# Kernel optimization log

Measured on AMD Instinct MI355X. Metric: run time of the kernel, lower is better.

The kernel has to match this reference:

```python
import jax, jax.numpy as jnp
import numpy as np

T, B = 2048, 128
H = 128          # hidden_size
QH = 1024        # query_hidden_size
NF = 32          # num_convolution_filters
K = 31           # convolution_filter_size (odd, same padding)


def setup_inputs() -> dict:
    key = jax.random.key(0)
    ks = jax.random.split(key, 10)
    encoded_tokens = jax.random.normal(ks[0], (T, B, H), dtype=jnp.float32)
    tokens_mask = jax.random.randint(ks[1], (B, T), 0, 2).astype(jnp.bool_)
    query = jax.random.normal(ks[2], (1, B, QH), dtype=jnp.float32)
    cumulative_alignment = jax.random.uniform(ks[3], (B, T), dtype=jnp.float32)
    # parameters
    conv_w = jax.random.normal(ks[4], (NF, 1, K), dtype=jnp.float32) * 0.1   # Conv1d weight [out,in,k]
    conv_b = jnp.zeros((NF,), dtype=jnp.float32)
    Wq = jax.random.normal(ks[5], (H, QH), dtype=jnp.float32) * (1.0 / np.sqrt(QH))
    bq = jnp.zeros((H,), dtype=jnp.float32)
    Wa = jax.random.normal(ks[6], (H, NF), dtype=jnp.float32) * (1.0 / np.sqrt(NF))
    ba = jnp.zeros((H,), dtype=jnp.float32)
    score_w = jax.random.normal(ks[7], (H,), dtype=jnp.float32) * (1.0 / np.sqrt(H))  # xavier-ish
    score_b = jnp.zeros((H,), dtype=jnp.float32)
    return dict(encoded_tokens=encoded_tokens, tokens_mask=tokens_mask, query=query,
                cumulative_alignment=cumulative_alignment, conv_w=conv_w, conv_b=conv_b,
                Wq=Wq, bq=bq, Wa=Wa, ba=ba, score_w=score_w, score_b=score_b)


def reference(encoded_tokens, tokens_mask, query, cumulative_alignment,
              conv_w, conv_b, Wq, bq, Wa, ba, score_w, score_b):
    # location features: Conv1d over cumulative alignment, same padding
    loc = jax.lax.conv_general_dilated(
        cumulative_alignment[:, None, :], conv_w,
        window_strides=(1,), padding=[((K - 1) // 2, (K - 1) // 2)],
        dimension_numbers=('NCH', 'OIH', 'NCH'))  # [B, NF, T]
    loc = loc + conv_b[None, :, None]
    loc = jnp.transpose(loc, (2, 0, 1))                        # [T, B, NF]
    loc = jnp.einsum('tbf,hf->tbh', loc, Wa) + ba              # [T, B, H]
    q = jnp.einsum('obq,hq->obh', query, Wq) + bq              # [1, B, H]
    # additive score: tanh of fused elementwise sum, then project to scalar
    score = jnp.tanh(encoded_tokens + q + loc + score_b)       # [T, B, H]
    s = jnp.einsum('tbh,h->bt', score, score_w)                # [B, T]
    s = jnp.where(tokens_mask, -jnp.inf, s)
    alignment = jax.nn.softmax(s, axis=1)                      # [B, T]
    context = jnp.einsum('bt,tbh->bh', alignment, encoded_tokens)  # [B, H]
    cumulative_alignment = cumulative_alignment + alignment
    return context, cumulative_alignment, alignment
```

## Files before the change

kernel.cpp:

```cpp
#include <hip/hip_runtime.h>
#include <stdint.h>

#define T_DIM 2048
#define B_DIM 128
#define H_DIM 128
#define QH_DIM 1024
#define NF 32
#define KW 31
#define TT 128
#define NTILE (T_DIM / TT)

#define NEG_INF (-__builtin_inff())

__device__ __forceinline__ float fast_tanh(float x) {
    float e = __expf(2.0f * x);
    return 1.0f - 2.0f * __builtin_amdgcn_rcpf(1.0f + e);
}

__global__ void k0_G(const float* __restrict__ Wa, const float* __restrict__ conv_w,
                     float* __restrict__ G) {
    int gid = blockIdx.x * blockDim.x + threadIdx.x;
    if (gid >= H_DIM * KW) return;
    int k = gid >> 7, h = gid & 127;
    float acc = 0.0f;
    #pragma unroll
    for (int f = 0; f < NF; ++f) acc = fmaf(Wa[h * NF + f], conv_w[f * KW + k], acc);
    G[gid] = acc;
}

__global__ __launch_bounds__(512)
void k1_query(const float* __restrict__ query, const float* __restrict__ Wq,
              const float* __restrict__ bq, const float* __restrict__ Wa,
              const float* __restrict__ conv_b, const float* __restrict__ ba,
              const float* __restrict__ score_b, float* __restrict__ qb) {
    const int b = blockIdx.x, tid = threadIdx.x;
    const int h = tid & 127, qtr = tid >> 7;
    __shared__ __align__(16) float qrow[QH_DIM];
    __shared__ float partial[512];
    for (int i = tid; i < QH_DIM; i += 512) qrow[i] = query[b * QH_DIM + i];
    __syncthreads();
    const float4* wq4 = (const float4*)(Wq + (size_t)h * QH_DIM + qtr * 256);
    const float4* q4 = (const float4*)(qrow + qtr * 256);
    float acc = 0.0f;
    #pragma unroll 4
    for (int j = 0; j < 64; ++j) {
        float4 w = wq4[j], q = q4[j];
        acc += w.x * q.x + w.y * q.y + w.z * q.z + w.w * q.w;
    }
    if (qtr == 0) {
        float cb = bq[h] + ba[h] + score_b[h];
        #pragma unroll
        for (int f = 0; f < NF; ++f) cb = fmaf(Wa[h * NF + f], conv_b[f], cb);
        acc += cb;
    }
    partial[tid] = acc;
    __syncthreads();
    if (tid < 128) qb[b * H_DIM + h] = partial[h] + partial[h + 128] + partial[h + 256] + partial[h + 384];
}

__global__ __launch_bounds__(256, 4)
void k2_score(const float* __restrict__ enc, const float* __restrict__ cum,
              const void* __restrict__ mask, const float* __restrict__ G,
              const float* __restrict__ qb, const float* __restrict__ score_w,
              float* __restrict__ s_out, float* __restrict__ o_part,
              float* __restrict__ ml_part) {
    const int b = blockIdx.x;
    const int tile = blockIdx.y;
    const int t0 = tile * TT;
    const int tid = threadIdx.x;
    const int l = tid & 63, wv = tid >> 6;

    __shared__ float Gs[KW * H_DIM];
    __shared__ float cw[TT + KW - 1];
    __shared__ float mbias[TT];
    __shared__ float oc[4][H_DIM];
    __shared__ float mwl[4], lwl[4];

    {
        uint32_t u = ((const uint32_t*)mask)[l];
        unsigned long long hi = __ballot(u > 1u);
        unsigned long long nf = __ballot(u != 0u && u != 0x3f800000u);
        int layout = (hi == 0ull) ? 0 : ((nf == 0ull) ? 2 : 1);
        if (tid < TT) {
            int idx = b * T_DIM + t0 + tid;
            bool m;
            if (layout == 0)      m = ((const int32_t*)mask)[idx] != 0;
            else if (layout == 1) m = ((const uint8_t*)mask)[idx] != 0;
            else                  m = ((const float*)mask)[idx] != 0.0f;
            mbias[tid] = m ? NEG_INF : 0.0f;
        }
    }
    for (int i = tid; i < KW * H_DIM; i += 256) Gs[i] = G[i];
    if (tid < TT + KW - 1) {
        int t = t0 - (KW / 2) + tid;
        cw[tid] = (t >= 0 && t < T_DIM) ? cum[b * T_DIM + t] : 0.0f;
    }
    __syncthreads();

    const float2 base = *(const float2*)(qb + b * H_DIM + 2 * l);
    const float2 w2 = *(const float2*)(score_w + 2 * l);

    float m_w = NEG_INF, l_w = 0.0f;
    float ox = 0.0f, oy = 0.0f;

    #pragma unroll
    for (int si = 0; si < 4; ++si) {
        const int cbase = wv * 32 + si * 8;
        float2 acc[8];
        #pragma unroll
        for (int it = 0; it < 8; ++it) acc[it] = base;

        {
            float tp[23];
            #pragma unroll
            for (int j = 0; j < 23; ++j) tp[j] = cw[cbase + j];
            #pragma unroll
            for (int k = 0; k < 16; ++k) {
                const float2 gk = *(const float2*)(&Gs[k * H_DIM + 2 * l]);
                #pragma unroll
                for (int it = 0; it < 8; ++it) {
                    acc[it].x = fmaf(gk.x, tp[k + it], acc[it].x);
                    acc[it].y = fmaf(gk.y, tp[k + it], acc[it].y);
                }
            }
        }
        {
            float tp[22];
            #pragma unroll
            for (int j = 0; j < 22; ++j) tp[j] = cw[cbase + 16 + j];
            #pragma unroll
            for (int k = 16; k < 31; ++k) {
                const float2 gk = *(const float2*)(&Gs[k * H_DIM + 2 * l]);
                #pragma unroll
                for (int it = 0; it < 8; ++it) {
                    acc[it].x = fmaf(gk.x, tp[k - 16 + it], acc[it].x);
                    acc[it].y = fmaf(gk.y, tp[k - 16 + it], acc[it].y);
                }
            }
        }

        const float* ep = enc + ((size_t)(t0 + cbase) * B_DIM + b) * H_DIM + 2 * l;
        float ex[8], ey[8], s_arr[8];
        #pragma unroll
        for (int it = 0; it < 8; ++it) {
            const float2 e2 = *(const float2*)(ep + (size_t)it * (B_DIM * H_DIM));
            ex[it] = e2.x; ey[it] = e2.y;
            float p = w2.x * fast_tanh(acc[it].x + e2.x)
                    + w2.y * fast_tanh(acc[it].y + e2.y);
            #pragma unroll
            for (int m = 32; m >= 1; m >>= 1) p += __shfl_xor(p, m, 64);
            s_arr[it] = p + mbias[cbase + it];
        }
        float sv = s_arr[0];
        #pragma unroll
        for (int it = 1; it < 8; ++it) sv = (l == it) ? s_arr[it] : sv;
        if (l < 8) s_out[b * T_DIM + t0 + cbase + l] = sv;
        float m8 = s_arr[0];
        #pragma unroll
        for (int it = 1; it < 8; ++it) m8 = fmaxf(m8, s_arr[it]);
        const float m_new = fmaxf(m_w, m8);
        const float m_use = (m_new == NEG_INF) ? 0.0f : m_new;
        const float alpha = __expf(m_w - m_use);
        float lsum = 0.0f, osx = 0.0f, osy = 0.0f;
        #pragma unroll
        for (int it = 0; it < 8; ++it) {
            const float e = __expf(s_arr[it] - m_use);
            lsum += e;
            osx = fmaf(e, ex[it], osx);
            osy = fmaf(e, ey[it], osy);
        }
        l_w = fmaf(l_w, alpha, lsum);
        ox = fmaf(ox, alpha, osx);
        oy = fmaf(oy, alpha, osy);
        m_w = m_new;
    }

    oc[wv][2 * l] = ox;
    oc[wv][2 * l + 1] = oy;
    if (l == 0) { mwl[wv] = m_w; lwl[wv] = l_w; }
    __syncthreads();
    if (tid < H_DIM) {
        const float mb = fmaxf(fmaxf(mwl[0], mwl[1]), fmaxf(mwl[2], mwl[3]));
        const float mu = (mb == NEG_INF) ? 0.0f : mb;
        const float b0 = __expf(mwl[0] - mu), b1 = __expf(mwl[1] - mu);
        const float b2 = __expf(mwl[2] - mu), b3 = __expf(mwl[3] - mu);
        const float o = oc[0][tid] * b0 + oc[1][tid] * b1 + oc[2][tid] * b2 + oc[3][tid] * b3;
        const int tbase = b * NTILE + tile;
        o_part[tbase * H_DIM + tid] = o;
        if (tid == 0) {
            ml_part[tbase * 2] = mb;
            ml_part[tbase * 2 + 1] = lwl[0] * b0 + lwl[1] * b1 + lwl[2] * b2 + lwl[3] * b3;
        }
    }
}

__global__ __launch_bounds__(256)
void k5_final(float* __restrict__ s_align, const float* __restrict__ cum_in,
              float* __restrict__ cum_out, const float* __restrict__ o_part,
              const float* __restrict__ ml_part, float* __restrict__ ctx) {
    const int b = blockIdx.x, tid = threadIdx.x;
    __shared__ float sm[NTILE], sl[NTILE], sb[NTILE];
    if (tid < NTILE) {
        sm[tid] = ml_part[(b * NTILE + tid) * 2];
        sl[tid] = ml_part[(b * NTILE + tid) * 2 + 1];
    }
    __syncthreads();
    float M = sm[0];
    #pragma unroll
    for (int i = 1; i < NTILE; ++i) M = fmaxf(M, sm[i]);
    const float M_use = (M == NEG_INF) ? 0.0f : M;
    if (tid < NTILE) sb[tid] = __expf(sm[tid] - M_use);
    __syncthreads();
    float L = 0.0f;
    #pragma unroll
    for (int i = 0; i < NTILE; ++i) L = fmaf(sl[i], sb[i], L);
    const float invL = 1.0f / L;
    if (tid < H_DIM) {
        float o = 0.0f;
        #pragma unroll
        for (int i = 0; i < NTILE; ++i)
            o = fmaf(o_part[(b * NTILE + i) * H_DIM + tid], sb[i], o);
        ctx[b * H_DIM + tid] = o * invL;
    }
    #pragma unroll
    for (int j = 0; j < 8; ++j) {
        const int idx = b * T_DIM + tid + j * 256;
        const float a = __expf(s_align[idx] - M_use) * invL;
        s_align[idx] = a;
        cum_out[idx] = cum_in[idx] + a;
    }
}

extern "C" void kernel_launch(void* const* d_in, const int* in_sizes, int n_in,
                              void* d_out, int out_size, void* d_ws, size_t ws_size,
                              hipStream_t stream) {
    const float* enc     = (const float*)d_in[0];
    const void*  mask    = d_in[1];
    const float* query   = (const float*)d_in[2];
    const float* cum     = (const float*)d_in[3];
    const float* conv_w  = (const float*)d_in[4];
    const float* conv_b  = (const float*)d_in[5];
    const float* Wq      = (const float*)d_in[6];
    const float* bq      = (const float*)d_in[7];
    const float* Wa      = (const float*)d_in[8];
    const float* ba      = (const float*)d_in[9];
    const float* score_w = (const float*)d_in[10];
    const float* score_b = (const float*)d_in[11];

    float* ctx_out   = (float*)d_out;
    float* cum_out   = ctx_out + B_DIM * H_DIM;
    float* align_out = cum_out + B_DIM * T_DIM;

    float* G      = (float*)d_ws;
    float* qb     = G + 4096;
    float* o_part = qb + B_DIM * H_DIM;
    float* ml     = o_part + B_DIM * NTILE * H_DIM;

    k0_G<<<16, 256, 0, stream>>>(Wa, conv_w, G);
    k1_query<<<B_DIM, 512, 0, stream>>>(query, Wq, bq, Wa, conv_b, ba, score_b, qb);
    k2_score<<<dim3(B_DIM, NTILE), 256, 0, stream>>>(enc, cum, mask, G, qb, score_w,
                                                     align_out, o_part, ml);
    k5_final<<<B_DIM, 256, 0, stream>>>(align_out, cum, cum_out, o_part, ml, ctx_out);
}
```

Baseline: 262.7 us.

## Precompute padded cumulative and mask bias, widen score tile, DPP wave reduction

Adds a prep kernel that writes a zero-padded copy of the cumulative alignment and a float mask bias to workspace, so the score kernel no longer stages them through shared memory or detects the mask layout per block. The score kernel now processes 16 timesteps per chunk instead of 8 and reuses 46 register-held conv inputs across all 31 taps. It prefetches all 16 encoder rows before the convolution, uses packed two-wide FMAs, and replaces the shuffle butterfly reduction with DPP row ops plus readlane. The cost is an extra kernel launch, extra global traffic for the padded buffers, and higher register pressure at 4 blocks per SIMD. The tp reads from global memory may also be less efficient than the earlier shared-memory reads.

```diff
diff --git a/kernel.cpp b/kernel.cpp
--- a/kernel.cpp
+++ b/kernel.cpp
@@ -9,12 +9,50 @@
 #define KW 31
 #define TT 128
 #define NTILE (T_DIM / TT)
+#define CPAD_ROW (T_DIM + 32)
 
 #define NEG_INF (-__builtin_inff())
+
+typedef float v2f __attribute__((ext_vector_type(2)));
 
 __device__ __forceinline__ float fast_tanh(float x) {
     float e = __expf(2.0f * x);
     return 1.0f - 2.0f * __builtin_amdgcn_rcpf(1.0f + e);
+}
+
+template <int CTRL>
+__device__ __forceinline__ float dpp_add(float x) {
+    int m = __builtin_amdgcn_update_dpp(0, __float_as_int(x), CTRL, 0xf, 0xf, true);
+    return x + __int_as_float(m);
+}
+__device__ __forceinline__ float wave_sum64(float x) {
+    x = dpp_add<0x111>(x);
+    x = dpp_add<0x112>(x);
+    x = dpp_add<0x114>(x);
+    x = dpp_add<0x118>(x);
+    x = dpp_add<0x142>(x);
+    x = dpp_add<0x143>(x);
+    return __int_as_float(__builtin_amdgcn_readlane(__float_as_int(x), 63));
+}
+
+__global__ __launch_bounds__(256)
+void k_prep(const float* __restrict__ cum, const void* __restrict__ mask,
+            float* __restrict__ cpad, float* __restrict__ mbias) {
+    const int gid = blockIdx.x * 256 + threadIdx.x;
+    const int b = gid >> 11, t = gid & 2047;
+    const int l = threadIdx.x & 63;
+    uint32_t u = ((const uint32_t*)mask)[l];
+    unsigned long long hi = __ballot(u > 1u);
+    unsigned long long nf = __ballot(u != 0u && u != 0x3f800000u);
+    int layout = (hi == 0ull) ? 0 : ((nf == 0ull) ? 2 : 1);
+    bool m;
+    if (layout == 0)      m = ((const int32_t*)mask)[gid] != 0;
+    else if (layout == 1) m = ((const uint8_t*)mask)[gid] != 0;
+    else                  m = ((const float*)mask)[gid] != 0.0f;
+    mbias[gid] = m ? NEG_INF : 0.0f;
+    cpad[b * CPAD_ROW + 16 + t] = cum[gid];
+    if (t < 16) cpad[b * CPAD_ROW + t] = 0.0f;
+    else if (t >= T_DIM - 16) cpad[b * CPAD_ROW + 32 + t] = 0.0f;
 }
 
 __global__ void k0_G(const float* __restrict__ Wa, const float* __restrict__ conv_w,
@@ -59,8 +97,8 @@
 }
 
 __global__ __launch_bounds__(256, 4)
-void k2_score(const float* __restrict__ enc, const float* __restrict__ cum,
-              const void* __restrict__ mask, const float* __restrict__ G,
+void k2_score(const float* __restrict__ enc, const float* __restrict__ cpad,
+              const float* __restrict__ mbias, const float* __restrict__ G,
               const float* __restrict__ qb, const float* __restrict__ score_w,
               float* __restrict__ s_out, float* __restrict__ o_part,
               float* __restrict__ ml_part) {
@@ -70,113 +108,82 @@
     const int tid = threadIdx.x;
     const int l = tid & 63, wv = tid >> 6;
 
-    __shared__ float Gs[KW * H_DIM];
-    __shared__ float cw[TT + KW - 1];
-    __shared__ float mbias[TT];
+    __shared__ v2f Gs[KW * 64];
     __shared__ float oc[4][H_DIM];
     __shared__ float mwl[4], lwl[4];
 
-    {
-        uint32_t u = ((const uint32_t*)mask)[l];
-        unsigned long long hi = __ballot(u > 1u);
-        unsigned long long nf = __ballot(u != 0u && u != 0x3f800000u);
-        int layout = (hi == 0ull) ? 0 : ((nf == 0ull) ? 2 : 1);
-        if (tid < TT) {
-            int idx = b * T_DIM + t0 + tid;
-            bool m;
-            if (layout == 0)      m = ((const int32_t*)mask)[idx] != 0;
-            else if (layout == 1) m = ((const uint8_t*)mask)[idx] != 0;
-            else                  m = ((const float*)mask)[idx] != 0.0f;
-            mbias[tid] = m ? NEG_INF : 0.0f;
-        }
-    }
-    for (int i = tid; i < KW * H_DIM; i += 256) Gs[i] = G[i];
-    if (tid < TT + KW - 1) {
-        int t = t0 - (KW / 2) + tid;
-        cw[tid] = (t >= 0 && t < T_DIM) ? cum[b * T_DIM + t] : 0.0f;
-    }
-    __syncthreads();
-
-    const float2 base = *(const float2*)(qb + b * H_DIM + 2 * l);
-    const float2 w2 = *(const float2*)(score_w + 2 * l);
+    for (int i = tid; i < KW * 64; i += 256) Gs[i] = ((const v2f*)G)[i];
+    __syncthreads();
+
+    const v2f base = *(const v2f*)(qb + b * H_DIM + 2 * l);
+    const v2f w2 = *(const v2f*)(score_w + 2 * l);
+    const float* crow = cpad + b * CPAD_ROW;
+    const float* mrow = mbias + b * T_DIM;
 
     float m_w = NEG_INF, l_w = 0.0f;
-    float ox = 0.0f, oy = 0.0f;
-
-    #pragma unroll
-    for (int si = 0; si < 4; ++si) {
-        const int cbase = wv * 32 + si * 8;
-        float2 acc[8];
-        #pragma unroll
-        for (int it = 0; it < 8; ++it) acc[it] = base;
-
-        {
-            float tp[23];
+    v2f o_w = {0.0f, 0.0f};
+
+    #pragma unroll
+    for (int c = 0; c < 2; ++c) {
+        const int tb = t0 + wv * 32 + c * 16;
+
+        float tp[46];
+        #pragma unroll
+        for (int j = 0; j < 46; ++j) tp[j] = crow[tb + j + 1];
+
+        const float* ep = enc + ((size_t)tb * B_DIM + b) * H_DIM + 2 * l;
+        v2f ee[16];
+        #pragma unroll
+        for (int it = 0; it < 16; ++it)
+            ee[it] = *(const v2f*)(ep + (size_t)it * (B_DIM * H_DIM));
+
+        v2f acc[16];
+        #pragma unroll
+        for (int it = 0; it < 16; ++it) acc[it] = base;
+        #pragma unroll
+        for (int k = 0; k < KW; ++k) {
+            const v2f g = Gs[k * 64 + l];
             #pragma unroll
-            for (int j = 0; j < 23; ++j) tp[j] = cw[cbase + j];
-            #pragma unroll
-            for (int k = 0; k < 16; ++k) {
-                const float2 gk = *(const float2*)(&Gs[k * H_DIM + 2 * l]);
-                #pragma unroll
-                for (int it = 0; it < 8; ++it) {
-                    acc[it].x = fmaf(gk.x, tp[k + it], acc[it].x);
-                    acc[it].y = fmaf(gk.y, tp[k + it], acc[it].y);
-                }
+            for (int it = 0; it < 16; ++it) {
+                const float cc = tp[k + it];
+                acc[it] = __builtin_elementwise_fma(g, (v2f){cc, cc}, acc[it]);
             }
         }
-        {
-            float tp[22];
-            #pragma unroll
-            for (int j = 0; j < 22; ++j) tp[j] = cw[cbase + 16 + j];
-            #pragma unroll
-            for (int k = 16; k < 31; ++k) {
-                const float2 gk = *(const float2*)(&Gs[k * H_DIM + 2 * l]);
-                #pragma unroll
-                for (int it = 0; it < 8; ++it) {
-                    acc[it].x = fmaf(gk.x, tp[k - 16 + it], acc[it].x);
-                    acc[it].y = fmaf(gk.y, tp[k - 16 + it], acc[it].y);
-                }
-            }
-        }
-
-        const float* ep = enc + ((size_t)(t0 + cbase) * B_DIM + b) * H_DIM + 2 * l;
-        float ex[8], ey[8], s_arr[8];
-        #pragma unroll
-        for (int it = 0; it < 8; ++it) {
-            const float2 e2 = *(const float2*)(ep + (size_t)it * (B_DIM * H_DIM));
-            ex[it] = e2.x; ey[it] = e2.y;
-            float p = w2.x * fast_tanh(acc[it].x + e2.x)
-                    + w2.y * fast_tanh(acc[it].y + e2.y);
-            #pragma unroll
-            for (int m = 32; m >= 1; m >>= 1) p += __shfl_xor(p, m, 64);
-            s_arr[it] = p + mbias[cbase + it];
-        }
-        float sv = s_arr[0];
-        #pragma unroll
-        for (int it = 1; it < 8; ++it) sv = (l == it) ? s_arr[it] : sv;
-        if (l < 8) s_out[b * T_DIM + t0 + cbase + l] = sv;
-        float m8 = s_arr[0];
-        #pragma unroll
-        for (int it = 1; it < 8; ++it) m8 = fmaxf(m8, s_arr[it]);
-        const float m_new = fmaxf(m_w, m8);
+
+        float su[16];
+        #pragma unroll
+        for (int it = 0; it < 16; ++it) {
+            v2f a = acc[it] + ee[it];
+            float p = w2.x * fast_tanh(a.x) + w2.y * fast_tanh(a.y);
+            su[it] = wave_sum64(p) + mrow[tb + it];
+        }
+
+        float sv = su[0];
+        #pragma unroll
+        for (int it = 1; it < 16; ++it) sv = (l == it) ? su[it] : sv;
+        if (l < 16) s_out[b * T_DIM + tb + l] = sv;
+
+        float mc = su[0];
+        #pragma unroll
+        for (int it = 1; it < 16; ++it) mc = fmaxf(mc, su[it]);
+        const float m_new = fmaxf(m_w, mc);
         const float m_use = (m_new == NEG_INF) ? 0.0f : m_new;
         const float alpha = __expf(m_w - m_use);
-        float lsum = 0.0f, osx = 0.0f, osy = 0.0f;
-        #pragma unroll
-        for (int it = 0; it < 8; ++it) {
-            const float e = __expf(s_arr[it] - m_use);
+        float lsum = 0.0f;
+        v2f osum = {0.0f, 0.0f};
+        #pragma unroll
+        for (int it = 0; it < 16; ++it) {
+            const float e = __expf(su[it] - m_use);
             lsum += e;
-            osx = fmaf(e, ex[it], osx);
-            osy = fmaf(e, ey[it], osy);
+            osum = __builtin_elementwise_fma((v2f){e, e}, ee[it], osum);
         }
         l_w = fmaf(l_w, alpha, lsum);
-        ox = fmaf(ox, alpha, osx);
-        oy = fmaf(oy, alpha, osy);
+        o_w = __builtin_elementwise_fma(o_w, (v2f){alpha, alpha}, osum);
         m_w = m_new;
     }
 
-    oc[wv][2 * l] = ox;
-    oc[wv][2 * l + 1] = oy;
+    oc[wv][2 * l] = o_w.x;
+    oc[wv][2 * l + 1] = o_w.y;
     if (l == 0) { mwl[wv] = m_w; lwl[wv] = l_w; }
     __syncthreads();
     if (tid < H_DIM) {
@@ -255,10 +262,13 @@
     float* qb     = G + 4096;
     float* o_part = qb + B_DIM * H_DIM;
     float* ml     = o_part + B_DIM * NTILE * H_DIM;
-
+    float* cpad   = ml + 4096;
+    float* mb     = cpad + B_DIM * CPAD_ROW;
+
+    k_prep<<<B_DIM * T_DIM / 256, 256, 0, stream>>>(cum, mask, cpad, mb);
     k0_G<<<16, 256, 0, stream>>>(Wa, conv_w, G);
     k1_query<<<B_DIM, 512, 0, stream>>>(query, Wq, bq, Wa, conv_b, ba, score_b, qb);
-    k2_score<<<dim3(B_DIM, NTILE), 256, 0, stream>>>(enc, cum, mask, G, qb, score_w,
+    k2_score<<<dim3(B_DIM, NTILE), 256, 0, stream>>>(enc, cpad, mb, G, qb, score_w,
                                                      align_out, o_part, ml);
     k5_final<<<B_DIM, 256, 0, stream>>>(align_out, cum, cum_out, o_part, ml, ctx_out);
 }
```

Result: no change. 264.5 us (+0.7%).

## Remap score kernel to one thread per timestep with LDS-staged encoder tiles

Applied to the files above, without the earlier changes.

The score kernel now assigns one timestep per thread over 256-step tiles instead of lanes across hidden units. Encoder chunks of 32 hidden units are staged through a padded shared-memory tile with register prefetch of the next chunk. The conv-projection weights are read from global memory in a pair-interleaved layout rather than copied to shared memory. Per-wave softmax reductions use DPP, and the context sum reloads the encoder rows in a second pass. This removes per-timestep cross-lane shuffle reductions and the shared G copy, at the cost of reading the encoder twice and adding more barriers and register pressure.

```diff
diff --git a/kernel.cpp b/kernel.cpp
--- a/kernel.cpp
+++ b/kernel.cpp
@@ -7,25 +7,51 @@
 #define QH_DIM 1024
 #define NF 32
 #define KW 31
-#define TT 128
-#define NTILE (T_DIM / TT)
+#define TB 256
+#define NTILE (T_DIM / TB)
+#define HC 32
+#define TROW 33
 
 #define NEG_INF (-__builtin_inff())
+
+typedef float v2f __attribute__((ext_vector_type(2)));
 
 __device__ __forceinline__ float fast_tanh(float x) {
     float e = __expf(2.0f * x);
     return 1.0f - 2.0f * __builtin_amdgcn_rcpf(1.0f + e);
 }
 
+template <int C>
+__device__ __forceinline__ float dpp_add(float x) {
+    int m = __builtin_amdgcn_update_dpp(0, __float_as_int(x), C, 0xf, 0xf, true);
+    return x + __int_as_float(m);
+}
+template <int C>
+__device__ __forceinline__ float dpp_max(float x) {
+    int m = __builtin_amdgcn_update_dpp(__float_as_int(x), __float_as_int(x), C, 0xf, 0xf, false);
+    return fmaxf(x, __int_as_float(m));
+}
+__device__ __forceinline__ float wave_sum64(float x) {
+    x = dpp_add<0x111>(x); x = dpp_add<0x112>(x); x = dpp_add<0x114>(x); x = dpp_add<0x118>(x);
+    x = dpp_add<0x142>(x); x = dpp_add<0x143>(x);
+    return __int_as_float(__builtin_amdgcn_readlane(__float_as_int(x), 63));
+}
+__device__ __forceinline__ float wave_max64(float x) {
+    x = dpp_max<0x111>(x); x = dpp_max<0x112>(x); x = dpp_max<0x114>(x); x = dpp_max<0x118>(x);
+    x = dpp_max<0x142>(x); x = dpp_max<0x143>(x);
+    return __int_as_float(__builtin_amdgcn_readlane(__float_as_int(x), 63));
+}
+
 __global__ void k0_G(const float* __restrict__ Wa, const float* __restrict__ conv_w,
-                     float* __restrict__ G) {
+                     float* __restrict__ Gp) {
     int gid = blockIdx.x * blockDim.x + threadIdx.x;
-    if (gid >= H_DIM * KW) return;
-    int k = gid >> 7, h = gid & 127;
+    if (gid >= 64 * 62) return;
+    int hp = gid / 62, r = gid - hp * 62;
+    int k = r >> 1, p = r & 1, h = 2 * hp + p;
     float acc = 0.0f;
     #pragma unroll
     for (int f = 0; f < NF; ++f) acc = fmaf(Wa[h * NF + f], conv_w[f * KW + k], acc);
-    G[gid] = acc;
+    Gp[gid] = acc;
 }
 
 __global__ __launch_bounds__(512)
@@ -59,124 +85,125 @@
 }
 
 __global__ __launch_bounds__(256, 4)
-void k2_score(const float* __restrict__ enc, const float* __restrict__ cum,
-              const void* __restrict__ mask, const float* __restrict__ G,
+void k2_fused(const float* __restrict__ enc, const float* __restrict__ cum,
+              const void* __restrict__ mask, const float* __restrict__ Gp,
               const float* __restrict__ qb, const float* __restrict__ score_w,
               float* __restrict__ s_out, float* __restrict__ o_part,
               float* __restrict__ ml_part) {
     const int b = blockIdx.x;
-    const int tile = blockIdx.y;
-    const int t0 = tile * TT;
+    const int tl = blockIdx.y;
+    const int t0 = tl * TB;
     const int tid = threadIdx.x;
     const int l = tid & 63, wv = tid >> 6;
 
-    __shared__ float Gs[KW * H_DIM];
-    __shared__ float cw[TT + KW - 1];
-    __shared__ float mbias[TT];
+    __shared__ float tile[TB][TROW];
+    __shared__ float cw[TB + 30];
+    __shared__ float esh[TB];
     __shared__ float oc[4][H_DIM];
     __shared__ float mwl[4], lwl[4];
 
+    float s;
     {
         uint32_t u = ((const uint32_t*)mask)[l];
         unsigned long long hi = __ballot(u > 1u);
         unsigned long long nf = __ballot(u != 0u && u != 0x3f800000u);
         int layout = (hi == 0ull) ? 0 : ((nf == 0ull) ? 2 : 1);
-        if (tid < TT) {
-            int idx = b * T_DIM + t0 + tid;
-            bool m;
-            if (layout == 0)      m = ((const int32_t*)mask)[idx] != 0;
-            else if (layout == 1) m = ((const uint8_t*)mask)[idx] != 0;
-            else                  m = ((const float*)mask)[idx] != 0.0f;
-            mbias[tid] = m ? NEG_INF : 0.0f;
-        }
-    }
-    for (int i = tid; i < KW * H_DIM; i += 256) Gs[i] = G[i];
-    if (tid < TT + KW - 1) {
-        int t = t0 - (KW / 2) + tid;
-        cw[tid] = (t >= 0 && t < T_DIM) ? cum[b * T_DIM + t] : 0.0f;
-    }
-    __syncthreads();
-
-    const float2 base = *(const float2*)(qb + b * H_DIM + 2 * l);
-    const float2 w2 = *(const float2*)(score_w + 2 * l);
-
-    float m_w = NEG_INF, l_w = 0.0f;
-    float ox = 0.0f, oy = 0.0f;
-
-    #pragma unroll
-    for (int si = 0; si < 4; ++si) {
-        const int cbase = wv * 32 + si * 8;
-        float2 acc[8];
-        #pragma unroll
-        for (int it = 0; it < 8; ++it) acc[it] = base;
-
-        {
-            float tp[23];
+        const int idx = b * T_DIM + t0 + tid;
+        bool m;
+        if (layout == 0)      m = ((const int32_t*)mask)[idx] != 0;
+        else if (layout == 1) m = ((const uint8_t*)mask)[idx] != 0;
+        else                  m = ((const float*)mask)[idx] != 0.0f;
+        s = m ? NEG_INF : 0.0f;
+    }
+
+    {
+        int tg = t0 - 15 + tid;
+        cw[tid] = (tg >= 0 && tg < T_DIM) ? cum[b * T_DIM + tg] : 0.0f;
+        if (tid < TB + 30 - 256) {
+            int j = 256 + tid;
+            int tg2 = t0 - 15 + j;
+            cw[j] = (tg2 >= 0 && tg2 < T_DIM) ? cum[b * T_DIM + tg2] : 0.0f;
+        }
+    }
+
+    const float* encb = enc + (size_t)t0 * (B_DIM * H_DIM) + b * H_DIM;
+    float4 pf[8];
+    #pragma unroll
+    for (int p = 0; p < 8; ++p) {
+        int g = p * 256 + tid;
+        int t = g >> 3, hq = g & 7;
+        pf[p] = *(const float4*)(encb + (size_t)t * (B_DIM * H_DIM) + 4 * hq);
+    }
+
+    __syncthreads();
+
+    float tp[KW];
+    #pragma unroll
+    for (int k = 0; k < KW; ++k) tp[k] = cw[tid + k];
+
+    #pragma unroll
+    for (int j = 0; j < 4; ++j) {
+        #pragma unroll
+        for (int p = 0; p < 8; ++p) {
+            int g = p * 256 + tid;
+            int t = g >> 3, hq = g & 7;
+            *(float4*)&tile[t][4 * hq] = pf[p];
+        }
+        __syncthreads();
+        if (j < 3) {
             #pragma unroll
-            for (int j = 0; j < 23; ++j) tp[j] = cw[cbase + j];
+            for (int p = 0; p < 8; ++p) {
+                int g = p * 256 + tid;
+                int t = g >> 3, hq = g & 7;
+                pf[p] = *(const float4*)(encb + (size_t)t * (B_DIM * H_DIM) + (j + 1) * HC + 4 * hq);
+            }
+        }
+        #pragma unroll
+        for (int hp = 0; hp < 16; ++hp) {
+            const int hg = j * HC + 2 * hp;
+            const float* gr = Gp + (j * 16 + hp) * 62;
+            v2f accA = { qb[b * H_DIM + hg], qb[b * H_DIM + hg + 1] };
+            v2f accB = { 0.0f, 0.0f };
             #pragma unroll
             for (int k = 0; k < 16; ++k) {
-                const float2 gk = *(const float2*)(&Gs[k * H_DIM + 2 * l]);
-                #pragma unroll
-                for (int it = 0; it < 8; ++it) {
-                    acc[it].x = fmaf(gk.x, tp[k + it], acc[it].x);
-                    acc[it].y = fmaf(gk.y, tp[k + it], acc[it].y);
-                }
+                const v2f g2 = *(const v2f*)(gr + 2 * k);
+                accA = __builtin_elementwise_fma(g2, (v2f){tp[k], tp[k]}, accA);
             }
-        }
-        {
-            float tp[22];
             #pragma unroll
-            for (int j = 0; j < 22; ++j) tp[j] = cw[cbase + 16 + j];
-            #pragma unroll
-            for (int k = 16; k < 31; ++k) {
-                const float2 gk = *(const float2*)(&Gs[k * H_DIM + 2 * l]);
-                #pragma unroll
-                for (int it = 0; it < 8; ++it) {
-                    acc[it].x = fmaf(gk.x, tp[k - 16 + it], acc[it].x);
-                    acc[it].y = fmaf(gk.y, tp[k - 16 + it], acc[it].y);
-                }
+            for (int k = 16; k < KW; ++k) {
+                const v2f g2 = *(const v2f*)(gr + 2 * k);
+                accB = __builtin_elementwise_fma(g2, (v2f){tp[k], tp[k]}, accB);
             }
-        }
-
-        const float* ep = enc + ((size_t)(t0 + cbase) * B_DIM + b) * H_DIM + 2 * l;
-        float ex[8], ey[8], s_arr[8];
-        #pragma unroll
-        for (int it = 0; it < 8; ++it) {
-            const float2 e2 = *(const float2*)(ep + (size_t)it * (B_DIM * H_DIM));
-            ex[it] = e2.x; ey[it] = e2.y;
-            float p = w2.x * fast_tanh(acc[it].x + e2.x)
-                    + w2.y * fast_tanh(acc[it].y + e2.y);
-            #pragma unroll
-            for (int m = 32; m >= 1; m >>= 1) p += __shfl_xor(p, m, 64);
-            s_arr[it] = p + mbias[cbase + it];
-        }
-        float sv = s_arr[0];
-        #pragma unroll
-        for (int it = 1; it < 8; ++it) sv = (l == it) ? s_arr[it] : sv;
-        if (l < 8) s_out[b * T_DIM + t0 + cbase + l] = sv;
-        float m8 = s_arr[0];
-        #pragma unroll
-        for (int it = 1; it < 8; ++it) m8 = fmaxf(m8, s_arr[it]);
-        const float m_new = fmaxf(m_w, m8);
-        const float m_use = (m_new == NEG_INF) ? 0.0f : m_new;
-        const float alpha = __expf(m_w - m_use);
-        float lsum = 0.0f, osx = 0.0f, osy = 0.0f;
-        #pragma unroll
-        for (int it = 0; it < 8; ++it) {
-            const float e = __expf(s_arr[it] - m_use);
-            lsum += e;
-            osx = fmaf(e, ex[it], osx);
-            osy = fmaf(e, ey[it], osy);
-        }
-        l_w = fmaf(l_w, alpha, lsum);
-        ox = fmaf(ox, alpha, osx);
-        oy = fmaf(oy, alpha, osy);
-        m_w = m_new;
-    }
-
-    oc[wv][2 * l] = ox;
-    oc[wv][2 * l + 1] = oy;
+            const v2f e2 = *(const v2f*)&tile[tid][2 * hp];
+            const v2f a2 = accA + accB + e2;
+            s += score_w[hg] * fast_tanh(a2.x) + score_w[hg + 1] * fast_tanh(a2.y);
+        }
+        __syncthreads();
+    }
+
+    s_out[b * T_DIM + t0 + tid] = s;
+
+    const float m_w = wave_max64(s);
+    const float m_use = (m_w == NEG_INF) ? 0.0f : m_w;
+    const float e = __expf(s - m_use);
+    const float l_w = wave_sum64(e);
+    esh[tid] = e;
+    __syncthreads();
+
+    const float* ep = enc + ((size_t)(t0 + wv * 64) * B_DIM + b) * H_DIM + 2 * l;
+    v2f oa = {0.0f, 0.0f}, ob = {0.0f, 0.0f};
+    #pragma unroll 8
+    for (int i = 0; i < 64; i += 2) {
+        const float e0 = esh[wv * 64 + i];
+        const float e1 = esh[wv * 64 + i + 1];
+        const v2f v0 = *(const v2f*)(ep + (size_t)i * (B_DIM * H_DIM));
+        const v2f v1 = *(const v2f*)(ep + (size_t)(i + 1) * (B_DIM * H_DIM));
+        oa = __builtin_elementwise_fma((v2f){e0, e0}, v0, oa);
+        ob = __builtin_elementwise_fma((v2f){e1, e1}, v1, ob);
+    }
+    const v2f o2 = oa + ob;
+    oc[wv][2 * l] = o2.x;
+    oc[wv][2 * l + 1] = o2.y;
     if (l == 0) { mwl[wv] = m_w; lwl[wv] = l_w; }
     __syncthreads();
     if (tid < H_DIM) {
@@ -185,11 +212,11 @@
         const float b0 = __expf(mwl[0] - mu), b1 = __expf(mwl[1] - mu);
         const float b2 = __expf(mwl[2] - mu), b3 = __expf(mwl[3] - mu);
         const float o = oc[0][tid] * b0 + oc[1][tid] * b1 + oc[2][tid] * b2 + oc[3][tid] * b3;
-        const int tbase = b * NTILE + tile;
-        o_part[tbase * H_DIM + tid] = o;
+        const int tb = b * NTILE + tl;
+        o_part[tb * H_DIM + tid] = o;
         if (tid == 0) {
-            ml_part[tbase * 2] = mb;
-            ml_part[tbase * 2 + 1] = lwl[0] * b0 + lwl[1] * b1 + lwl[2] * b2 + lwl[3] * b3;
+            ml_part[tb * 2] = mb;
+            ml_part[tb * 2 + 1] = lwl[0] * b0 + lwl[1] * b1 + lwl[2] * b2 + lwl[3] * b3;
         }
     }
 }
@@ -251,14 +278,14 @@
     float* cum_out   = ctx_out + B_DIM * H_DIM;
     float* align_out = cum_out + B_DIM * T_DIM;
 
-    float* G      = (float*)d_ws;
-    float* qb     = G + 4096;
+    float* Gp     = (float*)d_ws;
+    float* qb     = Gp + 4096;
     float* o_part = qb + B_DIM * H_DIM;
     float* ml     = o_part + B_DIM * NTILE * H_DIM;
 
-    k0_G<<<16, 256, 0, stream>>>(Wa, conv_w, G);
+    k0_G<<<16, 256, 0, stream>>>(Wa, conv_w, Gp);
     k1_query<<<B_DIM, 512, 0, stream>>>(query, Wq, bq, Wa, conv_b, ba, score_b, qb);
-    k2_score<<<dim3(B_DIM, NTILE), 256, 0, stream>>>(enc, cum, mask, G, qb, score_w,
+    k2_fused<<<dim3(B_DIM, NTILE), 256, 0, stream>>>(enc, cum, mask, Gp, qb, score_w,
                                                      align_out, o_part, ml);
     k5_final<<<B_DIM, 256, 0, stream>>>(align_out, cum, cum_out, o_part, ml, ctx_out);
 }
```

Result: slower. 290.5 us (+10.6%).
